# Performance work log

Hardware: AMD Instinct MI355X
Metric: run time of the kernel (lower is better)

Reference implementation:

```python
import jax, jax.numpy as jnp
import numpy as np

B, D = 65536, 1024
E, U, T = 10, 10, 2  # experts, expert units, tasks


def setup_inputs() -> dict:
    key = jax.random.key(0)
    ks = jax.random.split(key, 8)
    s = 0.02
    return {
        "x": jax.random.normal(ks[0], (B, D), dtype=jnp.float32),
        "show_index": jax.random.randint(ks[1], (B,), 0, 100),
        "st": jax.random.normal(ks[2], (B, 16), dtype=jnp.float32),
        "expert_w": jax.random.normal(ks[3], (E, D, U), dtype=jnp.float32) * s,
        "expert_b": jnp.zeros((E, U), dtype=jnp.float32),
        "gate_w": jax.random.normal(ks[4], (T, D, E), dtype=jnp.float32) * s,
        "gate_b": jnp.zeros((T, E), dtype=jnp.float32),
        "ctr_w": jax.random.normal(ks[5], (U, 1), dtype=jnp.float32) * s,
        "ctr_b": jnp.zeros((1,), dtype=jnp.float32),
        "cvr_w": jax.random.normal(ks[6], (U, 1), dtype=jnp.float32) * s,
        "cvr_b": jnp.zeros((1,), dtype=jnp.float32),
    }


def reference(x, show_index, st, expert_w, expert_b, gate_w, gate_b,
              ctr_w, ctr_b, cvr_w, cvr_b):
    # experts_output[b, u, e] = relu(x @ W_e + b_e)  (stacked on axis 2)
    experts_output = jax.nn.relu(
        jnp.einsum("bd,edu->bue", x, expert_w) + expert_b.T[None, :, :]
    )  # [B, U, E]
    # gates[b, t, e] = softmax over experts
    gates = jax.nn.softmax(
        jnp.einsum("bd,tde->bte", x, gate_w) + gate_b[None, :, :], axis=-1
    )  # [B, T, E]
    # weighted sum over experts for each task: [B, T, U]
    task_inputs = jnp.einsum("bue,bte->btu", experts_output, gates)
    ctr_logits = jax.nn.sigmoid(task_inputs[:, 0, :] @ ctr_w + ctr_b)  # [B, 1]
    cvr_logits = jax.nn.sigmoid(task_inputs[:, 1, :] @ cvr_w + cvr_b)  # [B, 1]
    return (ctr_logits, cvr_logits)
```

## Files before the change

### kernel.cpp

```cpp
#include <hip/hip_runtime.h>
#include <hip/hip_bf16.h>

#define B_ROWS 65536
#define D_DIM  1024
#define NC     120
#define MBLK   64
#define CSTR   121

typedef __attribute__((ext_vector_type(4))) float f32x4;
typedef __attribute__((ext_vector_type(8))) short bf16x8;

__device__ __forceinline__ unsigned short f2bf(float f) {
  union { float f; unsigned u; } v; v.f = f;
  unsigned r = v.u + 0x7FFFu + ((v.u >> 16) & 1u);
  return (unsigned short)(r >> 16);
}

__device__ __forceinline__ void gload_lds16(const short* g, short* l) {
  __builtin_amdgcn_global_load_lds(
      (const __attribute__((address_space(1))) void*)g,
      (__attribute__((address_space(3))) void*)l, 16, 0, 0);
}

__global__ __launch_bounds__(256) void pack_w(const float* __restrict__ ew,
                                              const float* __restrict__ gw,
                                              short* __restrict__ wt) {
  int idx = blockIdx.x * 256 + threadIdx.x;
  int c = idx >> 10, d = idx & 1023;
  float v = 0.f;
  if (c < 100) {
    int e = c / 10, u = c % 10;
    v = ew[(e * D_DIM + d) * 10 + u];
  } else if (c < NC) {
    int q = c - 100; int t = q / 10, e = q % 10;
    v = gw[(t * D_DIM + d) * 10 + e];
  }
  wt[c * D_DIM + d] = (short)f2bf(v);
}

union Smem {
  short Bq[2][8192];
  float C[MBLK * CSTR];
};

__global__ __launch_bounds__(256, 4) void mmoe_main(
    const float* __restrict__ x, const short* __restrict__ wt,
    const float* __restrict__ eb, const float* __restrict__ gb,
    const float* __restrict__ ctr_w, const float* __restrict__ ctr_b,
    const float* __restrict__ cvr_w, const float* __restrict__ cvr_b,
    float* __restrict__ out) {
  __shared__ Smem sm;
  const int tid  = threadIdx.x;
  const int wave = tid >> 6, lane = tid & 63;
  const int lhi  = lane >> 4, llo = lane & 15;
  const int m0   = blockIdx.x * MBLK;

  const float* xrow = x + (size_t)(m0 + wave * 16 + llo) * D_DIM + lhi * 8;

  f32x4 acc[8];
  #pragma unroll
  for (int i = 0; i < 8; ++i) acc[i] = (f32x4){0.f, 0.f, 0.f, 0.f};

  float4 pa[2][4];

  #pragma unroll
  for (int j = 0; j < 4; ++j) {
    const int slot = j * 256 + wave * 64 + lane;
    const int c = slot >> 3, p = slot & 7;
    const int g = p ^ (c & 7);
    gload_lds16(wt + c * D_DIM + g * 8,
                &sm.Bq[0][(j * 256 + wave * 64) * 8]);
  }
  pa[0][0] = *(const float4*)(xrow + 0);
  pa[0][1] = *(const float4*)(xrow + 4);
  pa[0][2] = *(const float4*)(xrow + 32);
  pa[0][3] = *(const float4*)(xrow + 36);
  __syncthreads();

  for (int ch = 0; ch < 16; ++ch) {
    const int cur = ch & 1;
    if (ch < 15) {
      const int k1 = (ch + 1) * 64;
      #pragma unroll
      for (int j = 0; j < 4; ++j) {
        const int slot = j * 256 + wave * 64 + lane;
        const int c = slot >> 3, p = slot & 7;
        const int g = p ^ (c & 7);
        gload_lds16(wt + c * D_DIM + k1 + g * 8,
                    &sm.Bq[cur ^ 1][(j * 256 + wave * 64) * 8]);
      }
      pa[cur ^ 1][0] = *(const float4*)(xrow + k1);
      pa[cur ^ 1][1] = *(const float4*)(xrow + k1 + 4);
      pa[cur ^ 1][2] = *(const float4*)(xrow + k1 + 32);
      pa[cur ^ 1][3] = *(const float4*)(xrow + k1 + 36);
    }
    bf16x8 af0, af1;
    {
      const float4 a = pa[cur][0], b = pa[cur][1];
      af0[0] = (short)f2bf(a.x); af0[1] = (short)f2bf(a.y);
      af0[2] = (short)f2bf(a.z); af0[3] = (short)f2bf(a.w);
      af0[4] = (short)f2bf(b.x); af0[5] = (short)f2bf(b.y);
      af0[6] = (short)f2bf(b.z); af0[7] = (short)f2bf(b.w);
      const float4 c2 = pa[cur][2], d2 = pa[cur][3];
      af1[0] = (short)f2bf(c2.x); af1[1] = (short)f2bf(c2.y);
      af1[2] = (short)f2bf(c2.z); af1[3] = (short)f2bf(c2.w);
      af1[4] = (short)f2bf(d2.x); af1[5] = (short)f2bf(d2.y);
      af1[6] = (short)f2bf(d2.z); af1[7] = (short)f2bf(d2.w);
    }
    const int swz = llo & 7;
    #pragma unroll
    for (int half = 0; half < 2; ++half) {
      const bf16x8 a = half ? af1 : af0;
      const int g0 = half * 4 + lhi;
      const int p  = g0 ^ swz;
      #pragma unroll
      for (int ct = 0; ct < 8; ++ct) {
        const bf16x8 bfr = *(const bf16x8*)&sm.Bq[cur][(ct * 16 + llo) * 64 + p * 8];
        acc[ct] = __builtin_amdgcn_mfma_f32_16x16x32_bf16(a, bfr, acc[ct], 0, 0, 0);
      }
    }
    __syncthreads();
  }

  #pragma unroll
  for (int ct = 0; ct < 8; ++ct) {
    const int col = ct * 16 + llo;
    if (col < NC) {
      #pragma unroll
      for (int r = 0; r < 4; ++r)
        sm.C[(wave * 16 + lhi * 4 + r) * CSTR + col] = acc[ct][r];
    }
  }
  __syncthreads();

  if (tid < 128) {
    const int task = tid >> 6, row = tid & 63;
    const float* crow = &sm.C[row * CSTR];
    const float* tw = task ? cvr_w : ctr_w;
    const float tb = task ? cvr_b[0] : ctr_b[0];
    float s[10];
    #pragma unroll
    for (int e = 0; e < 10; ++e) {
      float a = 0.f;
      #pragma unroll
      for (int u = 0; u < 10; ++u) {
        float v = fmaxf(crow[e * 10 + u] + eb[e * 10 + u], 0.f);
        a = fmaf(v, tw[u], a);
      }
      s[e] = a;
    }
    float gl[10], mx = -1e30f;
    #pragma unroll
    for (int e = 0; e < 10; ++e) {
      gl[e] = crow[100 + task * 10 + e] + gb[task * 10 + e];
      mx = fmaxf(mx, gl[e]);
    }
    float den = 0.f, num = 0.f;
    #pragma unroll
    for (int e = 0; e < 10; ++e) {
      float pz = __expf(gl[e] - mx);
      den += pz; num = fmaf(pz, s[e], num);
    }
    const float z = num / den + tb;
    out[task * B_ROWS + m0 + row] = 1.f / (1.f + __expf(-z));
  }
}

extern "C" void kernel_launch(void* const* d_in, const int* in_sizes, int n_in,
                              void* d_out, int out_size, void* d_ws, size_t ws_size,
                              hipStream_t stream) {
  const float* x     = (const float*)d_in[0];
  const float* ew    = (const float*)d_in[3];
  const float* eb    = (const float*)d_in[4];
  const float* gw    = (const float*)d_in[5];
  const float* gb    = (const float*)d_in[6];
  const float* ctr_w = (const float*)d_in[7];
  const float* ctr_b = (const float*)d_in[8];
  const float* cvr_w = (const float*)d_in[9];
  const float* cvr_b = (const float*)d_in[10];
  float* out = (float*)d_out;
  short* wt  = (short*)d_ws;

  pack_w<<<512, 256, 0, stream>>>(ew, gw, wt);
  mmoe_main<<<B_ROWS / MBLK, 256, 0, stream>>>(x, wt, eb, gb, ctr_w, ctr_b,
                                               cvr_w, cvr_b, out);
}
```

Baseline: 412.9 us.

## Load weight fragments directly from global into registers, drop LDS staging

Each wave now owns 32 rows (two 16-row MFMA tiles) and loads the B fragments from the packed weight buffer straight into registers with a register double buffer. This removes the LDS staging and the per-chunk block barriers, and each B fragment is reused across two row tiles. Blocks grow to 128 rows, the epilogue runs per wave on all 256 threads, and launch bounds drop to 2 blocks per CU. In exchange every wave rereads the weights from L2/L1 and register pressure rises, which may lower occupancy.

```diff
diff --git a/kernel.cpp b/kernel.cpp
--- a/kernel.cpp
+++ b/kernel.cpp
@@ -4,7 +4,6 @@
 #define B_ROWS 65536
 #define D_DIM  1024
 #define NC     120
-#define MBLK   64
 #define CSTR   121
 
 typedef __attribute__((ext_vector_type(4))) float f32x4;
@@ -16,10 +15,9 @@
   return (unsigned short)(r >> 16);
 }
 
-__device__ __forceinline__ void gload_lds16(const short* g, short* l) {
-  __builtin_amdgcn_global_load_lds(
-      (const __attribute__((address_space(1))) void*)g,
-      (__attribute__((address_space(3))) void*)l, 16, 0, 0);
+__device__ __forceinline__ short f2bfs(float f) {
+  __hip_bfloat16 h = __float2bfloat16(f);
+  return (short)__builtin_bit_cast(unsigned short, h);
 }
 
 __global__ __launch_bounds__(256) void pack_w(const float* __restrict__ ew,
@@ -38,104 +36,85 @@
   wt[c * D_DIM + d] = (short)f2bf(v);
 }
 
-union Smem {
-  short Bq[2][8192];
-  float C[MBLK * CSTR];
-};
-
-__global__ __launch_bounds__(256, 4) void mmoe_main(
+__global__ __launch_bounds__(256, 2) void mmoe_main(
     const float* __restrict__ x, const short* __restrict__ wt,
     const float* __restrict__ eb, const float* __restrict__ gb,
     const float* __restrict__ ctr_w, const float* __restrict__ ctr_b,
     const float* __restrict__ cvr_w, const float* __restrict__ cvr_b,
     float* __restrict__ out) {
-  __shared__ Smem sm;
+  __shared__ float C[4][32 * CSTR];
   const int tid  = threadIdx.x;
   const int wave = tid >> 6, lane = tid & 63;
   const int lhi  = lane >> 4, llo = lane & 15;
-  const int m0   = blockIdx.x * MBLK;
+  const int m0   = blockIdx.x * 128 + wave * 32;
 
-  const float* xrow = x + (size_t)(m0 + wave * 16 + llo) * D_DIM + lhi * 8;
+  const float* xr0 = x + (size_t)(m0 + llo) * D_DIM + lhi * 8;
+  const float* xr1 = xr0 + (size_t)16 * D_DIM;
+  const short* bb  = wt + llo * D_DIM + lhi * 8;
 
-  f32x4 acc[8];
+  f32x4 acc[2][8];
   #pragma unroll
-  for (int i = 0; i < 8; ++i) acc[i] = (f32x4){0.f, 0.f, 0.f, 0.f};
+  for (int rt = 0; rt < 2; ++rt)
+    #pragma unroll
+    for (int ct = 0; ct < 8; ++ct) acc[rt][ct] = (f32x4){0.f, 0.f, 0.f, 0.f};
 
-  float4 pa[2][4];
+  float4 pa[2][2][2];
+  uint4  pb[2][8];
 
+  pa[0][0][0] = *(const float4*)(xr0);
+  pa[0][0][1] = *(const float4*)(xr0 + 4);
+  pa[0][1][0] = *(const float4*)(xr1);
+  pa[0][1][1] = *(const float4*)(xr1 + 4);
   #pragma unroll
-  for (int j = 0; j < 4; ++j) {
-    const int slot = j * 256 + wave * 64 + lane;
-    const int c = slot >> 3, p = slot & 7;
-    const int g = p ^ (c & 7);
-    gload_lds16(wt + c * D_DIM + g * 8,
-                &sm.Bq[0][(j * 256 + wave * 64) * 8]);
-  }
-  pa[0][0] = *(const float4*)(xrow + 0);
-  pa[0][1] = *(const float4*)(xrow + 4);
-  pa[0][2] = *(const float4*)(xrow + 32);
-  pa[0][3] = *(const float4*)(xrow + 36);
-  __syncthreads();
+  for (int ct = 0; ct < 8; ++ct)
+    pb[0][ct] = *(const uint4*)(bb + ct * 16 * D_DIM);
 
-  for (int ch = 0; ch < 16; ++ch) {
-    const int cur = ch & 1;
-    if (ch < 15) {
-      const int k1 = (ch + 1) * 64;
-      #pragma unroll
-      for (int j = 0; j < 4; ++j) {
-        const int slot = j * 256 + wave * 64 + lane;
-        const int c = slot >> 3, p = slot & 7;
-        const int g = p ^ (c & 7);
-        gload_lds16(wt + c * D_DIM + k1 + g * 8,
-                    &sm.Bq[cur ^ 1][(j * 256 + wave * 64) * 8]);
-      }
-      pa[cur ^ 1][0] = *(const float4*)(xrow + k1);
-      pa[cur ^ 1][1] = *(const float4*)(xrow + k1 + 4);
-      pa[cur ^ 1][2] = *(const float4*)(xrow + k1 + 32);
-      pa[cur ^ 1][3] = *(const float4*)(xrow + k1 + 36);
+  #pragma unroll 2
+  for (int ks = 0; ks < 32; ++ks) {
+    const int cur = ks & 1, nxt = cur ^ 1;
+    const int kn = ((ks + 1) & 31) * 32;
+    pa[nxt][0][0] = *(const float4*)(xr0 + kn);
+    pa[nxt][0][1] = *(const float4*)(xr0 + kn + 4);
+    pa[nxt][1][0] = *(const float4*)(xr1 + kn);
+    pa[nxt][1][1] = *(const float4*)(xr1 + kn + 4);
+    #pragma unroll
+    for (int ct = 0; ct < 8; ++ct)
+      pb[nxt][ct] = *(const uint4*)(bb + ct * 16 * D_DIM + kn);
+
+    bf16x8 af[2];
+    #pragma unroll
+    for (int rt = 0; rt < 2; ++rt) {
+      const float4 a = pa[cur][rt][0], b = pa[cur][rt][1];
+      af[rt][0] = f2bfs(a.x); af[rt][1] = f2bfs(a.y);
+      af[rt][2] = f2bfs(a.z); af[rt][3] = f2bfs(a.w);
+      af[rt][4] = f2bfs(b.x); af[rt][5] = f2bfs(b.y);
+      af[rt][6] = f2bfs(b.z); af[rt][7] = f2bfs(b.w);
     }
-    bf16x8 af0, af1;
-    {
-      const float4 a = pa[cur][0], b = pa[cur][1];
-      af0[0] = (short)f2bf(a.x); af0[1] = (short)f2bf(a.y);
-      af0[2] = (short)f2bf(a.z); af0[3] = (short)f2bf(a.w);
-      af0[4] = (short)f2bf(b.x); af0[5] = (short)f2bf(b.y);
-      af0[6] = (short)f2bf(b.z); af0[7] = (short)f2bf(b.w);
-      const float4 c2 = pa[cur][2], d2 = pa[cur][3];
-      af1[0] = (short)f2bf(c2.x); af1[1] = (short)f2bf(c2.y);
-      af1[2] = (short)f2bf(c2.z); af1[3] = (short)f2bf(c2.w);
-      af1[4] = (short)f2bf(d2.x); af1[5] = (short)f2bf(d2.y);
-      af1[6] = (short)f2bf(d2.z); af1[7] = (short)f2bf(d2.w);
+    #pragma unroll
+    for (int ct = 0; ct < 8; ++ct) {
+      const bf16x8 bf = __builtin_bit_cast(bf16x8, pb[cur][ct]);
+      acc[0][ct] = __builtin_amdgcn_mfma_f32_16x16x32_bf16(af[0], bf, acc[0][ct], 0, 0, 0);
+      acc[1][ct] = __builtin_amdgcn_mfma_f32_16x16x32_bf16(af[1], bf, acc[1][ct], 0, 0, 0);
     }
-    const int swz = llo & 7;
-    #pragma unroll
-    for (int half = 0; half < 2; ++half) {
-      const bf16x8 a = half ? af1 : af0;
-      const int g0 = half * 4 + lhi;
-      const int p  = g0 ^ swz;
-      #pragma unroll
-      for (int ct = 0; ct < 8; ++ct) {
-        const bf16x8 bfr = *(const bf16x8*)&sm.Bq[cur][(ct * 16 + llo) * 64 + p * 8];
-        acc[ct] = __builtin_amdgcn_mfma_f32_16x16x32_bf16(a, bfr, acc[ct], 0, 0, 0);
-      }
-    }
-    __syncthreads();
   }
 
   #pragma unroll
-  for (int ct = 0; ct < 8; ++ct) {
-    const int col = ct * 16 + llo;
-    if (col < NC) {
-      #pragma unroll
-      for (int r = 0; r < 4; ++r)
-        sm.C[(wave * 16 + lhi * 4 + r) * CSTR + col] = acc[ct][r];
+  for (int rt = 0; rt < 2; ++rt) {
+    #pragma unroll
+    for (int ct = 0; ct < 8; ++ct) {
+      const int col = ct * 16 + llo;
+      if (col < NC) {
+        #pragma unroll
+        for (int r = 0; r < 4; ++r)
+          C[wave][(rt * 16 + lhi * 4 + r) * CSTR + col] = acc[rt][ct][r];
+      }
     }
   }
   __syncthreads();
 
-  if (tid < 128) {
-    const int task = tid >> 6, row = tid & 63;
-    const float* crow = &sm.C[row * CSTR];
+  {
+    const int task = lane >> 5, row = lane & 31;
+    const float* crow = &C[wave][row * CSTR];
     const float* tw = task ? cvr_w : ctr_w;
     const float tb = task ? cvr_b[0] : ctr_b[0];
     float s[10];
@@ -182,6 +161,6 @@
   short* wt  = (short*)d_ws;
 
   pack_w<<<512, 256, 0, stream>>>(ew, gw, wt);
-  mmoe_main<<<B_ROWS / MBLK, 256, 0, stream>>>(x, wt, eb, gb, ctr_w, ctr_b,
-                                               cvr_w, cvr_b, out);
+  mmoe_main<<<B_ROWS / 128, 256, 0, stream>>>(x, wt, eb, gb, ctr_w, ctr_b,
+                                              cvr_w, cvr_b, out);
 }
```

Measured after the change: 412.4 us. No clear change (-0.1%).
